# Optimization experiments

Hardware: AMD Instinct MI355X
Metric: run time of the kernel (lower is better)

Reference implementation:

```python
import jax, jax.numpy as jnp
import numpy as np

N_HEADS, D_MODEL, D_HEAD = 16, 1024, 64
INIT_STD = 0.02


def setup_inputs() -> dict:
    key = jax.random.key(0)
    ks = jax.random.split(key, 5)
    x = jax.random.normal(ks[0], (4, 2048, D_MODEL), dtype=jnp.float32)
    W_Q = jax.random.normal(ks[1], (N_HEADS, D_MODEL, D_HEAD), dtype=jnp.float32) * INIT_STD
    W_K = jax.random.normal(ks[2], (N_HEADS, D_MODEL, D_HEAD), dtype=jnp.float32) * INIT_STD
    W_V = jax.random.normal(ks[3], (N_HEADS, D_MODEL, D_HEAD), dtype=jnp.float32) * INIT_STD
    W_O = jax.random.normal(ks[4], (N_HEADS, D_HEAD, D_MODEL), dtype=jnp.float32) * INIT_STD
    b_Q = jnp.zeros((N_HEADS, D_HEAD), dtype=jnp.float32)
    b_K = jnp.zeros((N_HEADS, D_HEAD), dtype=jnp.float32)
    b_V = jnp.zeros((N_HEADS, D_HEAD), dtype=jnp.float32)
    b_O = jnp.zeros((D_MODEL,), dtype=jnp.float32)
    return {"normalized_resid_pre": x, "W_Q": W_Q, "W_K": W_K, "W_V": W_V,
            "W_O": W_O, "b_Q": b_Q, "b_K": b_K, "b_V": b_V, "b_O": b_O}


def reference(normalized_resid_pre, W_Q, W_K, W_V, W_O, b_Q, b_K, b_V, b_O):
    x = normalized_resid_pre  # [b, s, d_model]
    q = jnp.einsum('bsm,hmd->bshd', x, W_Q) + b_Q  # [b, s, h, d_head]
    k = jnp.einsum('bsm,hmd->bshd', x, W_K) + b_K
    v = jnp.einsum('bsm,hmd->bshd', x, W_V) + b_V
    scores = jnp.einsum('bqhd,bkhd->bhqk', q, k) / jnp.sqrt(jnp.float32(D_HEAD))
    S = x.shape[1]
    causal = jnp.tril(jnp.ones((S, S), dtype=bool))  # keep key_pos <= query_pos
    scores = jnp.where(causal, scores, jnp.finfo(scores.dtype).min)
    pattern = jax.nn.softmax(scores, axis=-1)  # [b, h, q, k]
    z = jnp.einsum('bhqk,bkhd->bqhd', pattern, v)
    attn_out = jnp.einsum('bqhd,hdm->bqm', z, W_O) + b_O
    return attn_out
```

## Files before the change

### kernel.cpp

```cpp
#include <hip/hip_runtime.h>
#include <hip/hip_bf16.h>
#include <math.h>

typedef __bf16 bf16_t;
typedef bf16_t bf16x8 __attribute__((ext_vector_type(8)));
typedef float f32x4 __attribute__((ext_vector_type(4)));

#define BB 4
#define SS 2048
#define HH 16
#define DMODEL 1024
#define DHEAD 64

#define QSCALE 0.18033688011112042f

__device__ inline unsigned short f2bf(float f) {
    union { __hip_bfloat16 h; unsigned short u; } cvt;
    cvt.h = __float2bfloat16(f);
    return cvt.u;
}

__device__ __forceinline__ void gll16(const unsigned short* g, unsigned short* l) {
    __builtin_amdgcn_global_load_lds(
        (const __attribute__((address_space(1))) unsigned int*)(g),
        (__attribute__((address_space(3))) unsigned int*)(l), 16, 0, 0);
}


__global__ void pack_all(const float* __restrict__ x,
                         const float* __restrict__ wq, const float* __restrict__ wk,
                         const float* __restrict__ wv, const float* __restrict__ wo,
                         unsigned short* __restrict__ xb, unsigned short* __restrict__ wqkv,
                         unsigned short* __restrict__ woT) {
    __shared__ float tile[64][65];
    const int t = threadIdx.x;
    const int bid = blockIdx.x;
    if (bid < 8192) {
        int i = bid * 256 + t;
        const float4 v = ((const float4*)x)[i];
        unsigned short o[4] = { f2bf(v.x), f2bf(v.y), f2bf(v.z), f2bf(v.w) };
        *(uint2*)(xb + 4 * (size_t)i) = *(uint2*)o;
        return;
    }
    const float* sbase;
    int sstride;
    unsigned short* dbase;
    if (bid < 8192 + 768) {
        int b2 = bid - 8192;
        int mat = b2 >> 8, rem = b2 & 255;
        int h = rem >> 4, mt = rem & 15;
        const float* wsrc = (mat == 0) ? wq : (mat == 1) ? wk : wv;
        sbase = wsrc + (h << 16) + ((mt * 64) << 6);
        sstride = 64;
        dbase = wqkv + (size_t)(mat * 1024 + h * 64) * 1024 + mt * 64;
    } else {
        int b3 = bid - 8960;
        int kt = b3 >> 4, nt = b3 & 15;
        sbase = wo + (size_t)(kt * 64) * 1024 + nt * 64;
        sstride = 1024;
        dbase = woT + (size_t)(nt * 64) * 1024 + kt * 64;
    }
    const int rr = t >> 4;
    const int c4 = (t & 15) * 4;
#pragma unroll
    for (int i = 0; i < 4; i++) {
        const int m = rr + 16 * i;
        const float4 v = *(const float4*)(sbase + (size_t)m * sstride + c4);
        tile[m][c4 + 0] = v.x;
        tile[m][c4 + 1] = v.y;
        tile[m][c4 + 2] = v.z;
        tile[m][c4 + 3] = v.w;
    }
    __syncthreads();
#pragma unroll
    for (int i = 0; i < 4; i++) {
        const int d = rr + 16 * i;
        unsigned short pk[4];
#pragma unroll
        for (int j = 0; j < 4; j++) pk[j] = f2bf(tile[c4 + j][d]);
        *(uint2*)(dbase + (size_t)d * 1024 + c4) = *(uint2*)pk;
    }
}


__global__ __launch_bounds__(256) void gemm_qkv(
    const unsigned short* __restrict__ xb,
    const unsigned short* __restrict__ wT,
    const float* __restrict__ bq, const float* __restrict__ bk, const float* __restrict__ bv,
    unsigned short* __restrict__ qws, unsigned short* __restrict__ kws,
    unsigned short* __restrict__ vtw)
{
    __shared__ __align__(16) unsigned short lA[128 * 64];
    __shared__ __align__(16) unsigned short lB[128 * 64];
    const int t = threadIdx.x;
    const int lane = t & 63;
    const int w = t >> 6;
    const int quad = lane >> 4;
    const int l15 = lane & 15;
    const int lo = l15 & 7;
    const int n0 = blockIdx.x * 128;
    const int m0 = blockIdx.y * 128;
    const int wm = (w >> 1) * 64;
    const int wn = (w & 1) * 64;
    const int mat = n0 >> 10;

    f32x4 acc[4][4] = {};

    const int sr8 = lane >> 3;
    const int g8 = lane & 7;
    const size_t soff = (size_t)(w * 8 + sr8) * 1024 + (size_t)(((g8 ^ sr8)) << 3);
    const unsigned short* Ab = xb + (size_t)m0 * 1024 + soff;
    const unsigned short* Bb = wT + (size_t)n0 * 1024 + soff;
    unsigned short* lAw = lA + (w * 8) * 64;
    unsigned short* lBw = lB + (w * 8) * 64;

    const int c0 = ((quad ^ lo)) << 3;
    const int c1 = (((4 | quad) ^ lo)) << 3;

    if (mat != 2) {
        for (int kt = 0; kt < 1024; kt += 64) {
            __syncthreads();
            gll16(Ab + kt,               lAw);
            gll16(Ab + 32 * 1024 + kt,   lAw + 32 * 64);
            gll16(Ab + 64 * 1024 + kt,   lAw + 64 * 64);
            gll16(Ab + 96 * 1024 + kt,   lAw + 96 * 64);
            gll16(Bb + kt,               lBw);
            gll16(Bb + 32 * 1024 + kt,   lBw + 32 * 64);
            gll16(Bb + 64 * 1024 + kt,   lBw + 64 * 64);
            gll16(Bb + 96 * 1024 + kt,   lBw + 96 * 64);
            __syncthreads();
            bf16x8 af[4][2], bfr[4][2];
#pragma unroll
            for (int i = 0; i < 4; i++) {
                af[i][0]  = *(const bf16x8*)(lA + (wm + i * 16 + l15) * 64 + c0);
                af[i][1]  = *(const bf16x8*)(lA + (wm + i * 16 + l15) * 64 + c1);
                bfr[i][0] = *(const bf16x8*)(lB + (wn + i * 16 + l15) * 64 + c0);
                bfr[i][1] = *(const bf16x8*)(lB + (wn + i * 16 + l15) * 64 + c1);
            }
#pragma unroll
            for (int i = 0; i < 4; i++)
#pragma unroll
                for (int j = 0; j < 4; j++) {
                    acc[i][j] = __builtin_amdgcn_mfma_f32_16x16x32_bf16(bfr[j][0], af[i][0], acc[i][j], 0, 0, 0);
                    acc[i][j] = __builtin_amdgcn_mfma_f32_16x16x32_bf16(bfr[j][1], af[i][1], acc[i][j], 0, 0, 0);
                }
        }
        const int b = m0 >> 11;
        const float* bias_p = (mat == 0) ? bq : bk;
        const float scale = (mat == 0) ? QSCALE : 1.0f;
        unsigned short* dst = (mat == 0) ? qws : kws;
#pragma unroll
        for (int j = 0; j < 4; j++) {
            const int noff = wn + j * 16 + quad * 4;
            const int h = noff >> 6;
            const int hglob = ((n0 & 1023) >> 6) + h;
            const int dbase = noff & 63;
            const float4 bv4 = *(const float4*)(bias_p + hglob * 64 + dbase);
            const float bias_r[4] = { bv4.x, bv4.y, bv4.z, bv4.w };
#pragma unroll
            for (int i = 0; i < 4; i++) {
                const int s = (m0 & 2047) + wm + i * 16 + l15;
                unsigned short pk[4];
#pragma unroll
                for (int r = 0; r < 4; r++) pk[r] = f2bf((acc[i][j][r] + bias_r[r]) * scale);
                *(uint2*)(dst + (size_t)((b * 16 + hglob) * 2048 + s) * 64 + dbase) = *(uint2*)pk;
            }
        }
    } else {
        for (int kt = 0; kt < 1024; kt += 64) {
            __syncthreads();
            gll16(Ab + kt,               lAw);
            gll16(Ab + 32 * 1024 + kt,   lAw + 32 * 64);
            gll16(Ab + 64 * 1024 + kt,   lAw + 64 * 64);
            gll16(Ab + 96 * 1024 + kt,   lAw + 96 * 64);
            gll16(Bb + kt,               lBw);
            gll16(Bb + 32 * 1024 + kt,   lBw + 32 * 64);
            gll16(Bb + 64 * 1024 + kt,   lBw + 64 * 64);
            gll16(Bb + 96 * 1024 + kt,   lBw + 96 * 64);
            __syncthreads();
            bf16x8 af[4][2], bfr[4][2];
#pragma unroll
            for (int i = 0; i < 4; i++) {
                af[i][0]  = *(const bf16x8*)(lA + (wm + i * 16 + l15) * 64 + c0);
                af[i][1]  = *(const bf16x8*)(lA + (wm + i * 16 + l15) * 64 + c1);
                bfr[i][0] = *(const bf16x8*)(lB + (wn + i * 16 + l15) * 64 + c0);
                bfr[i][1] = *(const bf16x8*)(lB + (wn + i * 16 + l15) * 64 + c1);
            }
#pragma unroll
            for (int i = 0; i < 4; i++)
#pragma unroll
                for (int j = 0; j < 4; j++) {
                    acc[i][j] = __builtin_amdgcn_mfma_f32_16x16x32_bf16(af[i][0], bfr[j][0], acc[i][j], 0, 0, 0);
                    acc[i][j] = __builtin_amdgcn_mfma_f32_16x16x32_bf16(af[i][1], bfr[j][1], acc[i][j], 0, 0, 0);
                }
        }
        const int b = m0 >> 11;
#pragma unroll
        for (int j = 0; j < 4; j++) {
            const int n1 = (n0 & 1023) + wn + j * 16 + l15;
            const int h = n1 >> 6, d = n1 & 63;
            const float bias = bv[h * 64 + d];
#pragma unroll
            for (int i = 0; i < 4; i++) {
                const int s0 = (m0 & 2047) + wm + i * 16 + quad * 4;
                unsigned short pk[4];
#pragma unroll
                for (int r = 0; r < 4; r++) pk[r] = f2bf(acc[i][j][r] + bias);
                *(uint2*)(vtw + ((size_t)(b * 16 + h) * 64 + d) * 2048 + s0) = *(uint2*)pk;
            }
        }
    }
}


__global__ __launch_bounds__(256) void gemm_out(
    const unsigned short* __restrict__ zb,
    const unsigned short* __restrict__ wT,
    const float* __restrict__ bo,
    float* __restrict__ out)
{
    __shared__ __align__(16) unsigned short lA[128 * 64];
    __shared__ __align__(16) unsigned short lB[128 * 64];
    const int t = threadIdx.x;
    const int lane = t & 63;
    const int w = t >> 6;
    const int quad = lane >> 4;
    const int l15 = lane & 15;
    const int lo = l15 & 7;
    const int n0 = blockIdx.x * 128;
    const int m0 = blockIdx.y * 128;
    const int wm = (w >> 1) * 64;
    const int wn = (w & 1) * 64;

    f32x4 acc[4][4] = {};

    const int sr8 = lane >> 3;
    const int g8 = lane & 7;
    const size_t soff = (size_t)(w * 8 + sr8) * 1024 + (size_t)(((g8 ^ sr8)) << 3);
    const unsigned short* Ab = zb + (size_t)m0 * 1024 + soff;
    const unsigned short* Bb = wT + (size_t)n0 * 1024 + soff;
    unsigned short* lAw = lA + (w * 8) * 64;
    unsigned short* lBw = lB + (w * 8) * 64;

    const int c0 = ((quad ^ lo)) << 3;
    const int c1 = (((4 | quad) ^ lo)) << 3;

    for (int kt = 0; kt < 1024; kt += 64) {
        __syncthreads();
        gll16(Ab + kt,               lAw);
        gll16(Ab + 32 * 1024 + kt,   lAw + 32 * 64);
        gll16(Ab + 64 * 1024 + kt,   lAw + 64 * 64);
        gll16(Ab + 96 * 1024 + kt,   lAw + 96 * 64);
        gll16(Bb + kt,               lBw);
        gll16(Bb + 32 * 1024 + kt,   lBw + 32 * 64);
        gll16(Bb + 64 * 1024 + kt,   lBw + 64 * 64);
        gll16(Bb + 96 * 1024 + kt,   lBw + 96 * 64);
        __syncthreads();
        bf16x8 af[4][2], bfr[4][2];
#pragma unroll
        for (int i = 0; i < 4; i++) {
            af[i][0]  = *(const bf16x8*)(lA + (wm + i * 16 + l15) * 64 + c0);
            af[i][1]  = *(const bf16x8*)(lA + (wm + i * 16 + l15) * 64 + c1);
            bfr[i][0] = *(const bf16x8*)(lB + (wn + i * 16 + l15) * 64 + c0);
            bfr[i][1] = *(const bf16x8*)(lB + (wn + i * 16 + l15) * 64 + c1);
        }
#pragma unroll
        for (int i = 0; i < 4; i++)
#pragma unroll
            for (int j = 0; j < 4; j++) {
                acc[i][j] = __builtin_amdgcn_mfma_f32_16x16x32_bf16(bfr[j][0], af[i][0], acc[i][j], 0, 0, 0);
                acc[i][j] = __builtin_amdgcn_mfma_f32_16x16x32_bf16(bfr[j][1], af[i][1], acc[i][j], 0, 0, 0);
            }
    }

#pragma unroll
    for (int j = 0; j < 4; j++) {
        const int nbase = n0 + wn + j * 16 + quad * 4;
        const float4 bv4 = *(const float4*)(bo + nbase);
#pragma unroll
        for (int i = 0; i < 4; i++) {
            const int s = m0 + wm + i * 16 + l15;
            float4 v;
            v.x = acc[i][j][0] + bv4.x;
            v.y = acc[i][j][1] + bv4.y;
            v.z = acc[i][j][2] + bv4.z;
            v.w = acc[i][j][3] + bv4.w;
            *(float4*)(out + (size_t)s * 1024 + nbase) = v;
        }
    }
}


__global__ __launch_bounds__(256) void attn3(
    const unsigned short* __restrict__ qws,
    const unsigned short* __restrict__ kws,
    const unsigned short* __restrict__ vtw,
    unsigned short* __restrict__ zb)
{
    __shared__ __align__(16) unsigned short Ks[64 * 64];
    __shared__ __align__(16) unsigned short Vs[64 * 64];
    __shared__ __align__(16) unsigned short Ps[4 * 16 * 64];

    const int t = threadIdx.x;
    const int lane = t & 63;
    const int w = t >> 6;
    const int quad = lane >> 4;
    const int l15 = lane & 15;
    const int lo = l15 & 7;

    const int qt = 31 - (blockIdx.x >> 6);
    const int bh = blockIdx.x & 63;
    const int q0 = qt * 64;
    const int qbase = q0 + w * 16;
    const size_t base = (size_t)bh * SS * DHEAD;
    const unsigned short* Q = qws + base;
    const unsigned short* K = kws + base;
    const unsigned short* Vt = vtw + base;

    bf16x8 qf0 = *(const bf16x8*)(Q + (size_t)(qbase + l15) * 64 + quad * 8);
    bf16x8 qf1 = *(const bf16x8*)(Q + (size_t)(qbase + l15) * 64 + 32 + quad * 8);

    f32x4 o[4] = {};
    float lsum = 0.f;
    unsigned short* Pw = Ps + w * 16 * 64;

    const int sr = t >> 2;
    const int g0 = t & 3;
    const int sw0 = ((g0 ^ (sr & 7)) << 3);
    const int sw1 = (((g0 + 4) ^ (sr & 7)) << 3);
    unsigned short* ksw = Ks + sr * 64;
    unsigned short* vsw = Vs + sr * 64;
    const unsigned short* Kg = K + (size_t)sr * 64 + g0 * 8;
    const unsigned short* Vg = Vt + (size_t)sr * 2048 + g0 * 8;

    const int gq0 = ((quad ^ lo) << 3);
    const int gq1 = (((quad + 4) ^ lo) << 3);

    unsigned short* pwr = Pw + l15 * 64;
    unsigned short* pws0 = pwr + (((0 + quad) ^ (lo << 1)) << 2);
    unsigned short* pws1 = pwr + (((4 + quad) ^ (lo << 1)) << 2);
    unsigned short* pws2 = pwr + (((8 + quad) ^ (lo << 1)) << 2);
    unsigned short* pws3 = pwr + (((12 + quad) ^ (lo << 1)) << 2);

    const int nch = qt + 1;

    uint4 kr0 = *(const uint4*)(Kg);
    uint4 kr1 = *(const uint4*)(Kg + 32);
    uint4 vr0 = *(const uint4*)(Vg);
    uint4 vr1 = *(const uint4*)(Vg + 32);

    for (int c = 0; c < nch; c++) {
        __builtin_amdgcn_sched_barrier(0);
        __builtin_amdgcn_s_barrier();
        *(uint4*)(ksw + sw0) = kr0;
        *(uint4*)(ksw + sw1) = kr1;
        *(uint4*)(vsw + sw0) = vr0;
        *(uint4*)(vsw + sw1) = vr1;
        if (c + 1 < nch) {
            const unsigned short* kp = Kg + (size_t)(c + 1) * 64 * 64;
            const unsigned short* vp = Vg + (size_t)(c + 1) * 64;
            kr0 = *(const uint4*)(kp);
            kr1 = *(const uint4*)(kp + 32);
            vr0 = *(const uint4*)(vp);
            vr1 = *(const uint4*)(vp + 32);
        }
        asm volatile("s_waitcnt lgkmcnt(0)" ::: "memory");
        __builtin_amdgcn_s_barrier();
        __builtin_amdgcn_sched_barrier(0);

        f32x4 s[4];
        __builtin_amdgcn_s_setprio(1);
#pragma unroll
        for (int sub = 0; sub < 4; sub++) {
            const unsigned short* kr = Ks + (sub * 16 + l15) * 64;
            bf16x8 kf0 = *(const bf16x8*)(kr + gq0);
            bf16x8 kf1 = *(const bf16x8*)(kr + gq1);
            f32x4 sv = {};
            sv = __builtin_amdgcn_mfma_f32_16x16x32_bf16(kf0, qf0, sv, 0, 0, 0);
            sv = __builtin_amdgcn_mfma_f32_16x16x32_bf16(kf1, qf1, sv, 0, 0, 0);
            s[sub] = sv;
        }
        __builtin_amdgcn_s_setprio(0);

        const int kb = c * 64;
        if (c == nch - 1) {
            const int qg = qbase + l15;
#pragma unroll
            for (int sub = 0; sub < 4; sub++) {
                const int k0 = kb + sub * 16 + quad * 4;
                unsigned short pk[4];
#pragma unroll
                for (int r = 0; r < 4; r++) {
                    float p = (k0 + r > qg) ? 0.f : exp2f(s[sub][r]);
                    lsum += p;
                    pk[r] = f2bf(p);
                }
                unsigned short* wp = (sub == 0) ? pws0 : (sub == 1) ? pws1 : (sub == 2) ? pws2 : pws3;
                *(uint2*)wp = *(uint2*)pk;
            }
        } else {
#pragma unroll
            for (int sub = 0; sub < 4; sub++) {
                unsigned short pk[4];
#pragma unroll
                for (int r = 0; r < 4; r++) {
                    float p = exp2f(s[sub][r]);
                    lsum += p;
                    pk[r] = f2bf(p);
                }
                unsigned short* wp = (sub == 0) ? pws0 : (sub == 1) ? pws1 : (sub == 2) ? pws2 : pws3;
                *(uint2*)wp = *(uint2*)pk;
            }
        }
        asm volatile("s_waitcnt lgkmcnt(0)" ::: "memory");
        bf16x8 pf0 = *(const bf16x8*)(Pw + l15 * 64 + gq0);
        bf16x8 pf1 = *(const bf16x8*)(Pw + l15 * 64 + gq1);
        __builtin_amdgcn_s_setprio(1);
#pragma unroll
        for (int dt = 0; dt < 4; dt++) {
            const unsigned short* vrp = Vs + (dt * 16 + l15) * 64;
            bf16x8 vf0 = *(const bf16x8*)(vrp + gq0);
            bf16x8 vf1 = *(const bf16x8*)(vrp + gq1);
            o[dt] = __builtin_amdgcn_mfma_f32_16x16x32_bf16(vf0, pf0, o[dt], 0, 0, 0);
            o[dt] = __builtin_amdgcn_mfma_f32_16x16x32_bf16(vf1, pf1, o[dt], 0, 0, 0);
        }
        __builtin_amdgcn_s_setprio(0);
    }

    float v = lsum;
    v += __shfl_xor(v, 16);
    v += __shfl_xor(v, 32);
    const float inv = 1.0f / v;

    const int b = bh >> 4, h = bh & 15;
    const int q = qbase + l15;
    unsigned short* zrow = zb + (size_t)(b * 2048 + q) * 1024 + h * 64 + quad * 4;
#pragma unroll
    for (int dt = 0; dt < 4; dt++) {
        unsigned short pk[4];
#pragma unroll
        for (int r = 0; r < 4; r++) pk[r] = f2bf(o[dt][r] * inv);
        *(uint2*)(zrow + dt * 16) = *(uint2*)pk;
    }
}


extern "C" void kernel_launch(void* const* d_in, const int* in_sizes, int n_in,
                              void* d_out, int out_size, void* d_ws, size_t ws_size,
                              hipStream_t stream) {
    const float* x  = (const float*)d_in[0];
    const float* WQ = (const float*)d_in[1];
    const float* WK = (const float*)d_in[2];
    const float* WV = (const float*)d_in[3];
    const float* WO = (const float*)d_in[4];
    const float* bQ = (const float*)d_in[5];
    const float* bK = (const float*)d_in[6];
    const float* bV = (const float*)d_in[7];
    const float* bO = (const float*)d_in[8];
    float* out = (float*)d_out;

    char* ws = (char*)d_ws;
    unsigned short* xb   = (unsigned short*)ws;
    unsigned short* wqkv = (unsigned short*)(ws + (16u << 20));
    unsigned short* woT  = (unsigned short*)(ws + (22u << 20));
    unsigned short* qws  = (unsigned short*)(ws + (24u << 20));
    unsigned short* kws  = (unsigned short*)(ws + (40u << 20));
    unsigned short* vtw  = (unsigned short*)(ws + (56u << 20));
    unsigned short* zbuf = xb;

    pack_all<<<9216, 256, 0, stream>>>(x, WQ, WK, WV, WO, xb, wqkv, woT);
    gemm_qkv<<<dim3(24, 64), 256, 0, stream>>>(xb, wqkv, bQ, bK, bV, qws, kws, vtw);
    attn3<<<2048, 256, 0, stream>>>(qws, kws, vtw, zbuf);
    gemm_out<<<dim3(8, 64), 256, 0, stream>>>(zbuf, woT, bO, out);
}
```

Before: 266.7 us.

## Double attention query tile to 128 rows with 8 waves sharing K/V tiles

The attention kernel now processes 128 query rows per block with 512 threads (8 waves), so each K/V chunk staged in shared memory is reused by twice as many waves and the grid is halved. Each thread now loads one 16-byte vector of K and V per chunk instead of two. Waves whose rows are entirely before a chunk skip compute with a continue, while the diagonal mask condition is generalised. The cost is more divergence in causal work across waves in the same block: early waves idle through the last chunk. Fewer blocks also reduces scheduling granularity.

Measured after the change: 254.7 us. -4.5%, faster.

```diff
diff --git a/kernel.cpp b/kernel.cpp
--- a/kernel.cpp
+++ b/kernel.cpp
@@ -291,7 +291,7 @@
 }
 
 
-__global__ __launch_bounds__(256) void attn3(
+__global__ __launch_bounds__(512) void attn3(
     const unsigned short* __restrict__ qws,
     const unsigned short* __restrict__ kws,
     const unsigned short* __restrict__ vtw,
@@ -299,7 +299,7 @@
 {
     __shared__ __align__(16) unsigned short Ks[64 * 64];
     __shared__ __align__(16) unsigned short Vs[64 * 64];
-    __shared__ __align__(16) unsigned short Ps[4 * 16 * 64];
+    __shared__ __align__(16) unsigned short Ps[8 * 16 * 64];
 
     const int t = threadIdx.x;
     const int lane = t & 63;
@@ -308,10 +308,9 @@
     const int l15 = lane & 15;
     const int lo = l15 & 7;
 
-    const int qt = 31 - (blockIdx.x >> 6);
+    const int qt = 15 - (blockIdx.x >> 6);
     const int bh = blockIdx.x & 63;
-    const int q0 = qt * 64;
-    const int qbase = q0 + w * 16;
+    const int qbase = qt * 128 + w * 16;
     const size_t base = (size_t)bh * SS * DHEAD;
     const unsigned short* Q = qws + base;
     const unsigned short* K = kws + base;
@@ -324,12 +323,11 @@
     float lsum = 0.f;
     unsigned short* Pw = Ps + w * 16 * 64;
 
-    const int sr = t >> 2;
-    const int g0 = t & 3;
-    const int sw0 = ((g0 ^ (sr & 7)) << 3);
-    const int sw1 = (((g0 + 4) ^ (sr & 7)) << 3);
-    unsigned short* ksw = Ks + sr * 64;
-    unsigned short* vsw = Vs + sr * 64;
+    const int sr = t >> 3;
+    const int g0 = t & 7;
+    const int swz = ((g0 ^ (sr & 7)) << 3);
+    unsigned short* ksw = Ks + sr * 64 + swz;
+    unsigned short* vsw = Vs + sr * 64 + swz;
     const unsigned short* Kg = K + (size_t)sr * 64 + g0 * 8;
     const unsigned short* Vg = Vt + (size_t)sr * 2048 + g0 * 8;
 
@@ -342,39 +340,34 @@
     unsigned short* pws2 = pwr + (((8 + quad) ^ (lo << 1)) << 2);
     unsigned short* pws3 = pwr + (((12 + quad) ^ (lo << 1)) << 2);
 
-    const int nch = qt + 1;
-
-    uint4 kr0 = *(const uint4*)(Kg);
-    uint4 kr1 = *(const uint4*)(Kg + 32);
-    uint4 vr0 = *(const uint4*)(Vg);
-    uint4 vr1 = *(const uint4*)(Vg + 32);
+    const int nch = 2 * qt + 2;
+
+    uint4 kr = *(const uint4*)(Kg);
+    uint4 vr = *(const uint4*)(Vg);
 
     for (int c = 0; c < nch; c++) {
         __builtin_amdgcn_sched_barrier(0);
         __builtin_amdgcn_s_barrier();
-        *(uint4*)(ksw + sw0) = kr0;
-        *(uint4*)(ksw + sw1) = kr1;
-        *(uint4*)(vsw + sw0) = vr0;
-        *(uint4*)(vsw + sw1) = vr1;
+        *(uint4*)ksw = kr;
+        *(uint4*)vsw = vr;
         if (c + 1 < nch) {
-            const unsigned short* kp = Kg + (size_t)(c + 1) * 64 * 64;
-            const unsigned short* vp = Vg + (size_t)(c + 1) * 64;
-            kr0 = *(const uint4*)(kp);
-            kr1 = *(const uint4*)(kp + 32);
-            vr0 = *(const uint4*)(vp);
-            vr1 = *(const uint4*)(vp + 32);
+            kr = *(const uint4*)(Kg + (size_t)(c + 1) * 64 * 64);
+            vr = *(const uint4*)(Vg + (size_t)(c + 1) * 64);
         }
         asm volatile("s_waitcnt lgkmcnt(0)" ::: "memory");
         __builtin_amdgcn_s_barrier();
         __builtin_amdgcn_sched_barrier(0);
 
+        const int kb = c * 64;
+        if (kb > qbase + 15) continue;
+
         f32x4 s[4];
         __builtin_amdgcn_s_setprio(1);
 #pragma unroll
         for (int sub = 0; sub < 4; sub++) {
-            const unsigned short* kr = Ks + (sub * 16 + l15) * 64;
-            bf16x8 kf0 = *(const bf16x8*)(kr + gq0);
-            bf16x8 kf1 = *(const bf16x8*)(kr + gq1);
+            const unsigned short* krow = Ks + (sub * 16 + l15) * 64;
+            bf16x8 kf0 = *(const bf16x8*)(krow + gq0);
+            bf16x8 kf1 = *(const bf16x8*)(krow + gq1);
             f32x4 sv = {};
             sv = __builtin_amdgcn_mfma_f32_16x16x32_bf16(kf0, qf0, sv, 0, 0, 0);
             sv = __builtin_amdgcn_mfma_f32_16x16x32_bf16(kf1, qf1, sv, 0, 0, 0);
@@ -382,8 +375,7 @@
         }
         __builtin_amdgcn_s_setprio(0);
 
-        const int kb = c * 64;
-        if (c == nch - 1) {
+        if (kb + 63 > qbase) {
             const int qg = qbase + l15;
 #pragma unroll
             for (int sub = 0; sub < 4; sub++) {
@@ -470,6 +462,6 @@
 
     pack_all<<<9216, 256, 0, stream>>>(x, WQ, WK, WV, WO, xb, wqkv, woT);
     gemm_qkv<<<dim3(24, 64), 256, 0, stream>>>(xb, wqkv, bQ, bK, bV, qws, kws, vtw);
-    attn3<<<2048, 256, 0, stream>>>(qws, kws, vtw, zbuf);
+    attn3<<<1024, 512, 0, stream>>>(qws, kws, vtw, zbuf);
     gemm_out<<<dim3(8, 64), 256, 0, stream>>>(zbuf, woT, bO, out);
 }
```
